# Performance work log

Measured on AMD Instinct MI355X. Metric: run time of the kernel, lower is better.

## Reference

```python
import jax, jax.numpy as jnp
import numpy as np

N_COMP = 16  # sedenion components

def _cd_table(n):
    """Cayley-Dickson basis multiplication table: e_i * e_j = sign[i,j] * e_{idx[i,j]}."""
    if n == 1:
        return np.array([[1]], dtype=np.int64), np.array([[0]], dtype=np.int64)
    m = n // 2
    s, k = _cd_table(m)
    conj = np.where(np.arange(m) == 0, 1, -1)  # conj(e_0)=e_0, conj(e_i)=-e_i
    S = np.zeros((n, n), dtype=np.int64)
    K = np.zeros((n, n), dtype=np.int64)
    for i in range(n):
        for j in range(n):
            if i < m and j < m:          # (a,0)(c,0) = (ac, 0)
                S[i, j] = s[i, j]; K[i, j] = k[i, j]
            elif i < m:                  # (a,0)(0,d) = (0, d a)
                q = j - m
                S[i, j] = s[q, i]; K[i, j] = m + k[q, i]
            elif j < m:                  # (0,b)(c,0) = (0, b c*)
                p = i - m
                S[i, j] = s[p, j] * conj[j]; K[i, j] = m + k[p, j]
            else:                        # (0,b)(0,d) = (-d* b, 0)
                p, q = i - m, j - m
                S[i, j] = -conj[q] * s[q, p]; K[i, j] = k[q, p]
    return S, K

SIGN, IDX = _cd_table(N_COMP)

def _sedenion_kernel(w_comp):
    """Assemble the (16n, 16n) real matrix of the sedenion linear map from 16 (n,n) component weights."""
    blocks = [[None] * N_COMP for _ in range(N_COMP)]
    for i in range(N_COMP):
        for j in range(N_COMP):
            blocks[j][int(IDX[i, j])] = float(SIGN[i, j]) * w_comp[i]
    return jnp.concatenate([jnp.concatenate(row, axis=1) for row in blocks], axis=0)


def setup_inputs() -> dict:
    key = jax.random.key(0)
    k1, k2, k3, k4 = jax.random.split(key, 4)
    B, C, H, W = 8, 96, 256, 256
    x = jax.random.normal(k1, (B, C, H, W), jnp.float32)
    w_comp = jax.random.normal(k2, (N_COMP, C, C), jnp.float32) * 0.02
    proj_w = jax.random.normal(k3, (C, C), jnp.float32) * 0.02
    proj_b = jax.random.normal(k4, (C,), jnp.float32) * 0.02
    return {"x": x, "w_comp": w_comp, "proj_w": proj_w, "proj_b": proj_b}


def reference(x, w_comp, proj_w, proj_b):
    B, C, H, W = x.shape
    h, w = H // 4, W // 4
    # get_window: 'b c (h s1) (w s2) -> b h w (s1 s2 c)' with s1=s2=4
    xw = x.reshape(B, C, h, 4, w, 4).transpose(0, 2, 4, 3, 5, 1).reshape(B, h, w, 16 * C)
    big = _sedenion_kernel(w_comp)          # (16C, 16C)
    y = xw @ big                            # sedenion linear on windowed features
    # reverse_window + 'b c h w -> b h w c' fused: (B,h,w,16C) -> (B,H,W,C)
    y = y.reshape(B, h, w, 4, 4, C).transpose(0, 1, 3, 2, 4, 5).reshape(B, H, W, C)
    y = jax.nn.gelu(y, approximate=False)   # nn.GELU (exact); dropouts are identity (p=0)
    y = y @ proj_w.T + proj_b               # nn.Linear(dim, dim)
    return y.transpose(0, 3, 1, 2)          # 'b h w c -> b c h w'
```

## Files before the change

kernel.cpp:

```cpp
#include <hip/hip_runtime.h>
#include <hip/hip_bf16.h>

typedef __attribute__((ext_vector_type(8))) short short8v;
typedef __attribute__((ext_vector_type(4))) float float4v;

struct SedTab { signed char sgn[256]; signed char idx[256]; };

__device__ inline unsigned short f2bf(float f) {
    __hip_bfloat16 h = __float2bfloat16(f);
    return *reinterpret_cast<unsigned short*>(&h);
}
__device__ inline float bf2f(unsigned short u) {
    union { unsigned int i; float f; } x; x.i = ((unsigned)u) << 16; return x.f;
}

#define GLOAD_LDS16(g, l) __builtin_amdgcn_global_load_lds( \
    (const __attribute__((address_space(1))) void*)(g), \
    (__attribute__((address_space(3))) void*)(l), 16, 0, 0)

#define VMCNT(n) asm volatile("s_waitcnt vmcnt(" #n ")" ::: "memory")

__global__ __launch_bounds__(256) void build_bigT(
    const float* __restrict__ w_comp, unsigned short* __restrict__ bigT, SedTab tab)
{
    int e = blockIdx.x * 256 + threadIdx.x;
    if (e >= 1536 * 1536) return;
    int n = e / 1536, k = e - n * 1536;
    int t_out = n / 96, c = n - t_out * 96;
    int t_in = k / 96, m = k - t_in * 96;
    int i = tab.idx[t_in * 16 + t_out];
    float s = (float)tab.sgn[t_in * 16 + t_out];
    float v = s * w_comp[(i * 96 + m) * 96 + c];
    bigT[e] = f2bf(v);
}

__global__ __launch_bounds__(256) void window_cast(
    const float* __restrict__ x, unsigned short* __restrict__ xw)
{
    __shared__ unsigned short lds[96][260];
    int blk = blockIdx.x;
    int s1 = blk & 3, hh = (blk >> 2) & 63, b = blk >> 8;
    const float* src = x + (size_t)b * 6291456 + (size_t)(4 * hh + s1) * 256;

    for (int i = threadIdx.x; i < 6144; i += 256) {
        int m = i >> 6;
        int q = (i & 63) << 2;
        float4 v = *(const float4*)(src + (size_t)m * 65536 + q);
        lds[m][q + 0] = f2bf(v.x);
        lds[m][q + 1] = f2bf(v.y);
        lds[m][q + 2] = f2bf(v.z);
        lds[m][q + 3] = f2bf(v.w);
    }
    __syncthreads();
    size_t rowbase = (size_t)((b * 64 + hh) * 64) * 1536 + (size_t)s1 * 384;
    for (int i = threadIdx.x; i < 3072; i += 256) {
        int ww = i / 48, g = i - ww * 48;
        int s2 = g / 12, mg = (g - s2 * 12) * 8;
        int qq = 4 * ww + s2;
        short8v pk;
        #pragma unroll
        for (int j = 0; j < 8; ++j) pk[j] = (short)lds[mg + j][qq];
        *(short8v*)(xw + rowbase + (size_t)ww * 1536 + s2 * 96 + mg) = pk;
    }
}

__global__ __launch_bounds__(512, 2) void gemm_sed8(
    const unsigned short* __restrict__ A,
    const unsigned short* __restrict__ Bt,
    unsigned short* __restrict__ Yg)
{
    __shared__ unsigned short As[3][256 * 64];
    __shared__ unsigned short Bs[2][256 * 64];
    const int t = threadIdx.x;
    const int lane = t & 63, w = t >> 6;
    const int wm = w >> 2, wn = w & 3;
    const int lr = lane & 15, lg = lane >> 4;

    const int bid = blockIdx.x;
    const int wg = (bid & 7) * 96 + (bid >> 3);
    const int nt = wg >> 7, mt = wg & 127;
    const int m0 = mt * 256, n0 = nt * 256;

    float4v acc[8][4];
    #pragma unroll
    for (int i = 0; i < 8; ++i)
        #pragma unroll
        for (int j = 0; j < 4; ++j) acc[i][j] = (float4v)0.0f;

    const int r0c = t >> 3,          r1c = (t + 512) >> 3;
    const int kc0 = ((t & 7) ^ (r0c & 7)) << 3;
    const int kc1 = (((t + 512) & 7) ^ (r1c & 7)) << 3;
    const unsigned short* gA0 = A  + (size_t)(m0 + r0c) * 1536 + kc0;
    const unsigned short* gA1 = A  + (size_t)(m0 + r1c) * 1536 + kc1;
    const unsigned short* gB0 = Bt + (size_t)(n0 + r0c) * 1536 + kc0;
    const unsigned short* gB1 = Bt + (size_t)(n0 + r1c) * 1536 + kc1;
    const int d0 = t * 16, d1 = (t + 512) * 16;

    auto stage2 = [&](const unsigned short* g0, const unsigned short* g1,
                      char* ldst, int ko, int half) {
        GLOAD_LDS16(g0 + ko + half * 196608, ldst + half * 16384 + d0);
        GLOAD_LDS16(g1 + ko + half * 196608, ldst + half * 16384 + d1);
    };

    char* a_rd = (char*)&As[0][0];
    char* a_md = (char*)&As[0][0] + 32768;
    char* a_wr = (char*)&As[0][0] + 65536;
    char* b_rd = (char*)&Bs[0][0];
    char* b_wr = (char*)&Bs[0][0] + 32768;

    stage2(gA0, gA1, a_rd, 0, 0);  stage2(gA0, gA1, a_rd, 0, 1);
    stage2(gB0, gB1, b_rd, 0, 0);  stage2(gB0, gB1, b_rd, 0, 1);
    stage2(gA0, gA1, a_md, 64, 0); stage2(gA0, gA1, a_md, 64, 1);
    VMCNT(4);
    __builtin_amdgcn_s_barrier();

    const int c0 = (lg * 8) ^ ((lr & 7) << 3);
    const int c1 = (32 + lg * 8) ^ ((lr & 7) << 3);
    const int arow0 = wm * 128 + lr;
    const int brow0 = wn * 64 + lr;

    int koB = 64, koA = 128;

    for (int kt = 0; kt < 24; ++kt) {
        const unsigned short* as = (const unsigned short*)a_rd;
        const unsigned short* bs = (const unsigned short*)b_rd;

        short8v a0[4], b0[4];
        #pragma unroll
        for (int mf = 0; mf < 4; ++mf)
            a0[mf] = *(const short8v*)(as + (arow0 + mf * 16) * 64 + c0);
        #pragma unroll
        for (int nf = 0; nf < 4; ++nf)
            b0[nf] = *(const short8v*)(bs + (brow0 + nf * 16) * 64 + c0);
        __builtin_amdgcn_sched_barrier(0);
        __builtin_amdgcn_s_barrier();
        if (kt < 23) stage2(gB0, gB1, b_wr, koB, 0);
        __builtin_amdgcn_s_setprio(1);
        #pragma unroll
        for (int mf = 0; mf < 4; ++mf)
            #pragma unroll
            for (int nf = 0; nf < 4; ++nf)
                acc[mf][nf] = __builtin_amdgcn_mfma_f32_16x16x32_bf16(
                    a0[mf], b0[nf], acc[mf][nf], 0, 0, 0);
        __builtin_amdgcn_s_setprio(0);

        short8v a1[4];
        #pragma unroll
        for (int mf = 0; mf < 4; ++mf)
            a1[mf] = *(const short8v*)(as + (arow0 + 64 + mf * 16) * 64 + c0);
        __builtin_amdgcn_sched_barrier(0);
        __builtin_amdgcn_s_barrier();
        if (kt < 23) stage2(gB0, gB1, b_wr, koB, 1);
        __builtin_amdgcn_s_setprio(1);
        #pragma unroll
        for (int mf = 0; mf < 4; ++mf)
            #pragma unroll
            for (int nf = 0; nf < 4; ++nf)
                acc[4 + mf][nf] = __builtin_amdgcn_mfma_f32_16x16x32_bf16(
                    a1[mf], b0[nf], acc[4 + mf][nf], 0, 0, 0);
        __builtin_amdgcn_s_setprio(0);

        short8v a2[4], b1[4];
        #pragma unroll
        for (int mf = 0; mf < 4; ++mf)
            a2[mf] = *(const short8v*)(as + (arow0 + mf * 16) * 64 + c1);
        #pragma unroll
        for (int nf = 0; nf < 4; ++nf)
            b1[nf] = *(const short8v*)(bs + (brow0 + nf * 16) * 64 + c1);
        __builtin_amdgcn_sched_barrier(0);
        __builtin_amdgcn_s_barrier();
        if (kt < 22) stage2(gA0, gA1, a_wr, koA, 0);
        __builtin_amdgcn_s_setprio(1);
        #pragma unroll
        for (int mf = 0; mf < 4; ++mf)
            #pragma unroll
            for (int nf = 0; nf < 4; ++nf)
                acc[mf][nf] = __builtin_amdgcn_mfma_f32_16x16x32_bf16(
                    a2[mf], b1[nf], acc[mf][nf], 0, 0, 0);
        __builtin_amdgcn_s_setprio(0);

        short8v a3[4];
        #pragma unroll
        for (int mf = 0; mf < 4; ++mf)
            a3[mf] = *(const short8v*)(as + (arow0 + 64 + mf * 16) * 64 + c1);
        if (kt < 22)       { VMCNT(2); }
        else if (kt == 22) { VMCNT(0); }
        __builtin_amdgcn_sched_barrier(0);
        __builtin_amdgcn_s_barrier();
        if (kt < 22) stage2(gA0, gA1, a_wr, koA, 1);
        __builtin_amdgcn_s_setprio(1);
        #pragma unroll
        for (int mf = 0; mf < 4; ++mf)
            #pragma unroll
            for (int nf = 0; nf < 4; ++nf)
                acc[4 + mf][nf] = __builtin_amdgcn_mfma_f32_16x16x32_bf16(
                    a3[mf], b1[nf], acc[4 + mf][nf], 0, 0, 0);
        __builtin_amdgcn_s_setprio(0);

        char* tmp = a_rd; a_rd = a_md; a_md = a_wr; a_wr = tmp;
        tmp = b_rd; b_rd = b_wr; b_wr = tmp;
        koB += 64; koA += 64;
    }

    #pragma unroll
    for (int mf = 0; mf < 8; ++mf) {
        #pragma unroll
        for (int r = 0; r < 4; ++r) {
            const int gm = m0 + wm * 128 + mf * 16 + lg * 4 + r;
            #pragma unroll
            for (int nf = 0; nf < 4; ++nf) {
                const int gn = n0 + wn * 64 + nf * 16 + lr;
                float v = acc[mf][nf][r];
                float g = 0.5f * v * (1.0f + erff(v * 0.70710678118654752f));
                Yg[(size_t)gm * 1536 + gn] = f2bf(g);
            }
        }
    }
}

__global__ __launch_bounds__(256, 2) void proj_mfma(
    const unsigned short* __restrict__ Yg,
    const float* __restrict__ pw, const float* __restrict__ pb,
    float* __restrict__ out)
{
    __shared__ unsigned short gys[256 * 104];
    __shared__ unsigned short pws[96 * 104];
    __shared__ float pbs[96];

    const int blk = blockIdx.x;
    const int s1 = blk & 3, hh = (blk >> 2) & 63, b = blk >> 8;
    const int t = threadIdx.x;
    const int lane = t & 63, w = t >> 6;
    const int lr = lane & 15;

    for (int i = t; i < 9216; i += 256) {
        int r = i / 96, c = i - r * 96;
        pws[r * 104 + c] = f2bf(pw[i]);
    }
    if (t < 96) pbs[t] = pb[t];

    size_t rowbase = (size_t)((b * 64 + hh) * 64) * 1536 + (size_t)s1 * 384;
    for (int i = t; i < 3072; i += 256) {
        int ww = i / 48, v = i - ww * 48;
        short8v pk = *(const short8v*)(Yg + rowbase + (size_t)ww * 1536 + v * 8);
        int s2 = v / 12;
        int c = (v - s2 * 12) * 8;
        int q = 4 * ww + s2;
        *(short8v*)(&gys[q * 104 + c]) = pk;
    }
    __syncthreads();

    float4v acc[6][4];
    #pragma unroll
    for (int i = 0; i < 6; ++i)
        #pragma unroll
        for (int j = 0; j < 4; ++j) acc[i][j] = (float4v)0.0f;

    #pragma unroll
    for (int ks = 0; ks < 3; ++ks) {
        const int lk = ks * 32 + ((lane >> 4) << 3);
        short8v af[6], bf[4];
        #pragma unroll
        for (int mf = 0; mf < 6; ++mf)
            af[mf] = *(const short8v*)(&pws[(mf * 16 + lr) * 104 + lk]);
        #pragma unroll
        for (int nf = 0; nf < 4; ++nf)
            bf[nf] = *(const short8v*)(&gys[(w * 64 + nf * 16 + lr) * 104 + lk]);
        #pragma unroll
        for (int mf = 0; mf < 6; ++mf)
            #pragma unroll
            for (int nf = 0; nf < 4; ++nf)
                acc[mf][nf] = __builtin_amdgcn_mfma_f32_16x16x32_bf16(
                    af[mf], bf[nf], acc[mf][nf], 0, 0, 0);
    }

    const int p = 4 * hh + s1;
    const size_t obase = (size_t)b * 6291456 + (size_t)p * 256;
    #pragma unroll
    for (int mf = 0; mf < 6; ++mf) {
        #pragma unroll
        for (int r = 0; r < 4; ++r) {
            const int c = mf * 16 + (lane >> 4) * 4 + r;
            const float bias = pbs[c];
            #pragma unroll
            for (int nf = 0; nf < 4; ++nf) {
                const int q = w * 64 + nf * 16 + lr;
                out[obase + (size_t)c * 65536 + q] = acc[mf][nf][r] + bias;
            }
        }
    }
}

static void cd_table(int n, int* S, int* K) {
    if (n == 1) { S[0] = 1; K[0] = 0; return; }
    int m = n / 2;
    int s[64], k[64];
    cd_table(m, s, k);
    for (int i = 0; i < n; ++i) {
        for (int j = 0; j < n; ++j) {
            if (i < m && j < m) { S[i*n+j] = s[i*m+j]; K[i*n+j] = k[i*m+j]; }
            else if (i < m) { int q = j - m; S[i*n+j] = s[q*m+i]; K[i*n+j] = m + k[q*m+i]; }
            else if (j < m) { int p = i - m; int cj = (j == 0) ? 1 : -1;
                              S[i*n+j] = s[p*m+j] * cj; K[i*n+j] = m + k[p*m+j]; }
            else { int p = i - m, q = j - m; int cq = (q == 0) ? 1 : -1;
                   S[i*n+j] = -cq * s[q*m+p]; K[i*n+j] = k[q*m+p]; }
        }
    }
}

extern "C" void kernel_launch(void* const* d_in, const int* in_sizes, int n_in,
                              void* d_out, int out_size, void* d_ws, size_t ws_size,
                              hipStream_t stream) {
    const float* x      = (const float*)d_in[0];
    const float* w_comp = (const float*)d_in[1];
    const float* proj_w = (const float*)d_in[2];
    const float* proj_b = (const float*)d_in[3];
    float* out = (float*)d_out;

    unsigned short* BigT = (unsigned short*)d_ws;
    unsigned short* Yg   = (unsigned short*)((char*)d_ws + 4718592);
    unsigned short* Xw   = (unsigned short*)d_out;

    int S16[256], K16[256];
    cd_table(16, S16, K16);
    SedTab tab;
    for (int i = 0; i < 16; ++i)
        for (int j = 0; j < 16; ++j) {
            int k = K16[i * 16 + j];
            tab.idx[j * 16 + k] = (signed char)i;
            tab.sgn[j * 16 + k] = (signed char)S16[i * 16 + j];
        }

    hipLaunchKernelGGL(build_bigT, dim3(9216), dim3(256), 0, stream, w_comp, BigT, tab);
    hipLaunchKernelGGL(window_cast, dim3(2048), dim3(256), 0, stream, x, Xw);
    hipLaunchKernelGGL(gemm_sed8, dim3(768), dim3(512), 0, stream, Xw, BigT, Yg);
    hipLaunchKernelGGL(proj_mfma, dim3(2048), dim3(256), 0, stream, Yg, proj_w, proj_b, out);
}
```

Baseline: 333.0 us.

## Fuse projection GEMM into sedenion GEMM epilogue with 128x384 tiles

Retiles the main GEMM from 256x256 to 128x384 tiles so that each block owns whole 96-channel groups (four spatial sub-positions). The GELU output then stays in LDS, and the 96x96 projection plus bias runs in the same kernel. This removes the bf16 intermediate Y round-trip through global memory and one kernel launch. The cost is a larger LDS footprint (144KB), a different operand-prefetch schedule, each block reloading proj_w, and the windowed input moving from the output buffer into the workspace.

```diff
diff --git a/kernel.cpp b/kernel.cpp
--- a/kernel.cpp
+++ b/kernel.cpp
@@ -9,9 +9,6 @@
 __device__ inline unsigned short f2bf(float f) {
     __hip_bfloat16 h = __float2bfloat16(f);
     return *reinterpret_cast<unsigned short*>(&h);
-}
-__device__ inline float bf2f(unsigned short u) {
-    union { unsigned int i; float f; } x; x.i = ((unsigned)u) << 16; return x.f;
 }
 
 #define GLOAD_LDS16(g, l) __builtin_amdgcn_global_load_lds( \
@@ -64,137 +61,135 @@
     }
 }
 
-__global__ __launch_bounds__(512, 2) void gemm_sed8(
+__global__ __launch_bounds__(512, 2) void gemm_fused(
     const unsigned short* __restrict__ A,
     const unsigned short* __restrict__ Bt,
-    unsigned short* __restrict__ Yg)
+    const float* __restrict__ pw, const float* __restrict__ pb,
+    float* __restrict__ out)
 {
-    __shared__ unsigned short As[3][256 * 64];
-    __shared__ unsigned short Bs[2][256 * 64];
+    __shared__ __attribute__((aligned(16))) char smem[147456];
     const int t = threadIdx.x;
     const int lane = t & 63, w = t >> 6;
     const int wm = w >> 2, wn = w & 3;
     const int lr = lane & 15, lg = lane >> 4;
 
     const int bid = blockIdx.x;
-    const int wg = (bid & 7) * 96 + (bid >> 3);
-    const int nt = wg >> 7, mt = wg & 127;
-    const int m0 = mt * 256, n0 = nt * 256;
-
-    float4v acc[8][4];
-    #pragma unroll
-    for (int i = 0; i < 8; ++i)
-        #pragma unroll
-        for (int j = 0; j < 4; ++j) acc[i][j] = (float4v)0.0f;
-
-    const int r0c = t >> 3,          r1c = (t + 512) >> 3;
-    const int kc0 = ((t & 7) ^ (r0c & 7)) << 3;
-    const int kc1 = (((t + 512) & 7) ^ (r1c & 7)) << 3;
-    const unsigned short* gA0 = A  + (size_t)(m0 + r0c) * 1536 + kc0;
-    const unsigned short* gA1 = A  + (size_t)(m0 + r1c) * 1536 + kc1;
-    const unsigned short* gB0 = Bt + (size_t)(n0 + r0c) * 1536 + kc0;
-    const unsigned short* gB1 = Bt + (size_t)(n0 + r1c) * 1536 + kc1;
-    const int d0 = t * 16, d1 = (t + 512) * 16;
-
-    auto stage2 = [&](const unsigned short* g0, const unsigned short* g1,
-                      char* ldst, int ko, int half) {
-        GLOAD_LDS16(g0 + ko + half * 196608, ldst + half * 16384 + d0);
-        GLOAD_LDS16(g1 + ko + half * 196608, ldst + half * 16384 + d1);
+    const int wg = (bid & 7) * 128 + (bid >> 3);
+    const int nt = wg >> 8, mt = wg & 255;
+    const int m0 = mt * 128, n0 = nt * 384;
+
+    float4v acc[4][6];
+    #pragma unroll
+    for (int i = 0; i < 4; ++i)
+        #pragma unroll
+        for (int j = 0; j < 6; ++j) acc[i][j] = (float4v)0.0f;
+
+    const int rA = t >> 3;
+    const int kc = ((t & 7) ^ (rA & 7)) << 3;
+    const unsigned short* gA = A  + (size_t)(m0 + rA) * 1536 + kc;
+    const unsigned short* gB = Bt + (size_t)(n0 + rA) * 1536 + kc;
+    const int dst = t * 16;
+
+    auto stageA = [&](char* s, int ko) {
+        GLOAD_LDS16(gA + ko,             s + dst);
+        GLOAD_LDS16(gA + ko + 64 * 1536, s + dst + 8192);
     };
-
-    char* a_rd = (char*)&As[0][0];
-    char* a_md = (char*)&As[0][0] + 32768;
-    char* a_wr = (char*)&As[0][0] + 65536;
-    char* b_rd = (char*)&Bs[0][0];
-    char* b_wr = (char*)&Bs[0][0] + 32768;
-
-    stage2(gA0, gA1, a_rd, 0, 0);  stage2(gA0, gA1, a_rd, 0, 1);
-    stage2(gB0, gB1, b_rd, 0, 0);  stage2(gB0, gB1, b_rd, 0, 1);
-    stage2(gA0, gA1, a_md, 64, 0); stage2(gA0, gA1, a_md, 64, 1);
-    VMCNT(4);
+    auto stageB = [&](char* s, int ko) {
+        #pragma unroll
+        for (int i = 0; i < 6; ++i)
+            GLOAD_LDS16(gB + ko + (size_t)i * 64 * 1536, s + dst + i * 8192);
+    };
+
+    char* a_rd = smem;          char* a_md = smem + 16384; char* a_wr = smem + 32768;
+    char* b_rd = smem + 49152;  char* b_wr = smem + 98304;
+
+    stageA(a_rd, 0); stageB(b_rd, 0); stageA(a_md, 64);
+    VMCNT(2);
     __builtin_amdgcn_s_barrier();
 
     const int c0 = (lg * 8) ^ ((lr & 7) << 3);
     const int c1 = (32 + lg * 8) ^ ((lr & 7) << 3);
-    const int arow0 = wm * 128 + lr;
-    const int brow0 = wn * 64 + lr;
+    const int ar = wm * 64 + lr;
+    const int br = wn * 96 + lr;
+
+    short8v aE[4], aO[4], b0[3], b1[3], b2[3], b3[3];
+    {
+        const unsigned short* as = (const unsigned short*)a_rd;
+        const unsigned short* bs = (const unsigned short*)b_rd;
+        #pragma unroll
+        for (int mf = 0; mf < 4; ++mf) aE[mf] = *(const short8v*)(as + (ar + mf * 16) * 64 + c0);
+        #pragma unroll
+        for (int j = 0; j < 3; ++j)    b0[j]  = *(const short8v*)(bs + (br + j * 16) * 64 + c0);
+        __builtin_amdgcn_sched_barrier(0);
+    }
 
     int koB = 64, koA = 128;
-
     for (int kt = 0; kt < 24; ++kt) {
         const unsigned short* as = (const unsigned short*)a_rd;
         const unsigned short* bs = (const unsigned short*)b_rd;
 
-        short8v a0[4], b0[4];
+        if (kt < 23) stageB(b_wr, koB);
+        __builtin_amdgcn_s_barrier();
+        #pragma unroll
+        for (int j = 0; j < 3; ++j) b1[j] = *(const short8v*)(bs + (br + (3 + j) * 16) * 64 + c0);
+        __builtin_amdgcn_sched_barrier(0);
+        __builtin_amdgcn_s_setprio(1);
         #pragma unroll
         for (int mf = 0; mf < 4; ++mf)
-            a0[mf] = *(const short8v*)(as + (arow0 + mf * 16) * 64 + c0);
-        #pragma unroll
-        for (int nf = 0; nf < 4; ++nf)
-            b0[nf] = *(const short8v*)(bs + (brow0 + nf * 16) * 64 + c0);
-        __builtin_amdgcn_sched_barrier(0);
+            #pragma unroll
+            for (int nf = 0; nf < 3; ++nf)
+                acc[mf][nf] = __builtin_amdgcn_mfma_f32_16x16x32_bf16(
+                    aE[mf], b0[nf], acc[mf][nf], 0, 0, 0);
+        __builtin_amdgcn_s_setprio(0);
+
         __builtin_amdgcn_s_barrier();
-        if (kt < 23) stage2(gB0, gB1, b_wr, koB, 0);
+        #pragma unroll
+        for (int mf = 0; mf < 4; ++mf) aO[mf] = *(const short8v*)(as + (ar + mf * 16) * 64 + c1);
+        #pragma unroll
+        for (int j = 0; j < 3; ++j)    b2[j]  = *(const short8v*)(bs + (br + j * 16) * 64 + c1);
+        __builtin_amdgcn_sched_barrier(0);
         __builtin_amdgcn_s_setprio(1);
         #pragma unroll
         for (int mf = 0; mf < 4; ++mf)
             #pragma unroll
-            for (int nf = 0; nf < 4; ++nf)
+            for (int nf = 0; nf < 3; ++nf)
+                acc[mf][3 + nf] = __builtin_amdgcn_mfma_f32_16x16x32_bf16(
+                    aE[mf], b1[nf], acc[mf][3 + nf], 0, 0, 0);
+        __builtin_amdgcn_s_setprio(0);
+
+        if (kt < 22) stageA(a_wr, koA);
+        __builtin_amdgcn_s_barrier();
+        #pragma unroll
+        for (int j = 0; j < 3; ++j) b3[j] = *(const short8v*)(bs + (br + (3 + j) * 16) * 64 + c1);
+        __builtin_amdgcn_sched_barrier(0);
+        __builtin_amdgcn_s_setprio(1);
+        #pragma unroll
+        for (int mf = 0; mf < 4; ++mf)
+            #pragma unroll
+            for (int nf = 0; nf < 3; ++nf)
                 acc[mf][nf] = __builtin_amdgcn_mfma_f32_16x16x32_bf16(
-                    a0[mf], b0[nf], acc[mf][nf], 0, 0, 0);
+                    aO[mf], b2[nf], acc[mf][nf], 0, 0, 0);
         __builtin_amdgcn_s_setprio(0);
 
-        short8v a1[4];
-        #pragma unroll
-        for (int mf = 0; mf < 4; ++mf)
-            a1[mf] = *(const short8v*)(as + (arow0 + 64 + mf * 16) * 64 + c0);
-        __builtin_amdgcn_sched_barrier(0);
-        __builtin_amdgcn_s_barrier();
-        if (kt < 23) stage2(gB0, gB1, b_wr, koB, 1);
-        __builtin_amdgcn_s_setprio(1);
-        #pragma unroll
-        for (int mf = 0; mf < 4; ++mf)
-            #pragma unroll
-            for (int nf = 0; nf < 4; ++nf)
-                acc[4 + mf][nf] = __builtin_amdgcn_mfma_f32_16x16x32_bf16(
-                    a1[mf], b0[nf], acc[4 + mf][nf], 0, 0, 0);
-        __builtin_amdgcn_s_setprio(0);
-
-        short8v a2[4], b1[4];
-        #pragma unroll
-        for (int mf = 0; mf < 4; ++mf)
-            a2[mf] = *(const short8v*)(as + (arow0 + mf * 16) * 64 + c1);
-        #pragma unroll
-        for (int nf = 0; nf < 4; ++nf)
-            b1[nf] = *(const short8v*)(bs + (brow0 + nf * 16) * 64 + c1);
-        __builtin_amdgcn_sched_barrier(0);
-        __builtin_amdgcn_s_barrier();
-        if (kt < 22) stage2(gA0, gA1, a_wr, koA, 0);
-        __builtin_amdgcn_s_setprio(1);
-        #pragma unroll
-        for (int mf = 0; mf < 4; ++mf)
-            #pragma unroll
-            for (int nf = 0; nf < 4; ++nf)
-                acc[mf][nf] = __builtin_amdgcn_mfma_f32_16x16x32_bf16(
-                    a2[mf], b1[nf], acc[mf][nf], 0, 0, 0);
-        __builtin_amdgcn_s_setprio(0);
-
-        short8v a3[4];
-        #pragma unroll
-        for (int mf = 0; mf < 4; ++mf)
-            a3[mf] = *(const short8v*)(as + (arow0 + 64 + mf * 16) * 64 + c1);
         if (kt < 22)       { VMCNT(2); }
         else if (kt == 22) { VMCNT(0); }
-        __builtin_amdgcn_sched_barrier(0);
         __builtin_amdgcn_s_barrier();
-        if (kt < 22) stage2(gA0, gA1, a_wr, koA, 1);
+        if (kt < 23) {
+            const unsigned short* asn = (const unsigned short*)a_md;
+            const unsigned short* bsn = (const unsigned short*)b_wr;
+            #pragma unroll
+            for (int mf = 0; mf < 4; ++mf) aE[mf] = *(const short8v*)(asn + (ar + mf * 16) * 64 + c0);
+            #pragma unroll
+            for (int j = 0; j < 3; ++j)    b0[j]  = *(const short8v*)(bsn + (br + j * 16) * 64 + c0);
+        }
+        __builtin_amdgcn_sched_barrier(0);
         __builtin_amdgcn_s_setprio(1);
         #pragma unroll
         for (int mf = 0; mf < 4; ++mf)
             #pragma unroll
-            for (int nf = 0; nf < 4; ++nf)
-                acc[4 + mf][nf] = __builtin_amdgcn_mfma_f32_16x16x32_bf16(
-                    a3[mf], b1[nf], acc[4 + mf][nf], 0, 0, 0);
+            for (int nf = 0; nf < 3; ++nf)
+                acc[mf][3 + nf] = __builtin_amdgcn_mfma_f32_16x16x32_bf16(
+                    aO[mf], b3[nf], acc[mf][3 + nf], 0, 0, 0);
         __builtin_amdgcn_s_setprio(0);
 
         char* tmp = a_rd; a_rd = a_md; a_md = a_wr; a_wr = tmp;
@@ -202,90 +197,73 @@
         koB += 64; koA += 64;
     }
 
-    #pragma unroll
-    for (int mf = 0; mf < 8; ++mf) {
+    __syncthreads();
+
+    unsigned short* yl  = (unsigned short*)smem;
+    unsigned short* pwl = (unsigned short*)(smem + 106496);
+    float*          pbl = (float*)(smem + 126464);
+
+    for (int i = t; i < 9216; i += 512) {
+        int r = i / 96, c = i - r * 96;
+        pwl[r * 104 + c] = f2bf(pw[i]);
+    }
+    if (t < 96) pbl[t] = pb[t];
+
+    #pragma unroll
+    for (int mf = 0; mf < 4; ++mf) {
         #pragma unroll
         for (int r = 0; r < 4; ++r) {
-            const int gm = m0 + wm * 128 + mf * 16 + lg * 4 + r;
-            #pragma unroll
-            for (int nf = 0; nf < 4; ++nf) {
-                const int gn = n0 + wn * 64 + nf * 16 + lr;
+            const int ww = mf * 16 + lg * 4 + r;
+            const int pos = wm * 256 + 4 * ww + wn;
+            #pragma unroll
+            for (int nf = 0; nf < 6; ++nf) {
                 float v = acc[mf][nf][r];
                 float g = 0.5f * v * (1.0f + erff(v * 0.70710678118654752f));
-                Yg[(size_t)gm * 1536 + gn] = f2bf(g);
+                yl[pos * 104 + nf * 16 + lr] = f2bf(g);
             }
         }
     }
-}
-
-__global__ __launch_bounds__(256, 2) void proj_mfma(
-    const unsigned short* __restrict__ Yg,
-    const float* __restrict__ pw, const float* __restrict__ pb,
-    float* __restrict__ out)
-{
-    __shared__ unsigned short gys[256 * 104];
-    __shared__ unsigned short pws[96 * 104];
-    __shared__ float pbs[96];
-
-    const int blk = blockIdx.x;
-    const int s1 = blk & 3, hh = (blk >> 2) & 63, b = blk >> 8;
-    const int t = threadIdx.x;
-    const int lane = t & 63, w = t >> 6;
-    const int lr = lane & 15;
-
-    for (int i = t; i < 9216; i += 256) {
-        int r = i / 96, c = i - r * 96;
-        pws[r * 104 + c] = f2bf(pw[i]);
-    }
-    if (t < 96) pbs[t] = pb[t];
-
-    size_t rowbase = (size_t)((b * 64 + hh) * 64) * 1536 + (size_t)s1 * 384;
-    for (int i = t; i < 3072; i += 256) {
-        int ww = i / 48, v = i - ww * 48;
-        short8v pk = *(const short8v*)(Yg + rowbase + (size_t)ww * 1536 + v * 8);
-        int s2 = v / 12;
-        int c = (v - s2 * 12) * 8;
-        int q = 4 * ww + s2;
-        *(short8v*)(&gys[q * 104 + c]) = pk;
-    }
     __syncthreads();
 
-    float4v acc[6][4];
+    float4v pacc[6][4];
     #pragma unroll
     for (int i = 0; i < 6; ++i)
         #pragma unroll
-        for (int j = 0; j < 4; ++j) acc[i][j] = (float4v)0.0f;
-
+        for (int j = 0; j < 4; ++j) pacc[i][j] = (float4v)0.0f;
+
+    const int posr = w * 64 + lr;
     #pragma unroll
     for (int ks = 0; ks < 3; ++ks) {
-        const int lk = ks * 32 + ((lane >> 4) << 3);
-        short8v af[6], bf[4];
-        #pragma unroll
-        for (int mf = 0; mf < 6; ++mf)
-            af[mf] = *(const short8v*)(&pws[(mf * 16 + lr) * 104 + lk]);
-        #pragma unroll
-        for (int nf = 0; nf < 4; ++nf)
-            bf[nf] = *(const short8v*)(&gys[(w * 64 + nf * 16 + lr) * 104 + lk]);
-        #pragma unroll
-        for (int mf = 0; mf < 6; ++mf)
-            #pragma unroll
-            for (int nf = 0; nf < 4; ++nf)
-                acc[mf][nf] = __builtin_amdgcn_mfma_f32_16x16x32_bf16(
-                    af[mf], bf[nf], acc[mf][nf], 0, 0, 0);
-    }
-
-    const int p = 4 * hh + s1;
+        const int ck = ks * 32 + lg * 8;
+        short8v pf[6], yf[4];
+        #pragma unroll
+        for (int mf2 = 0; mf2 < 6; ++mf2)
+            pf[mf2] = *(const short8v*)(pwl + (mf2 * 16 + lr) * 104 + ck);
+        #pragma unroll
+        for (int nf2 = 0; nf2 < 4; ++nf2)
+            yf[nf2] = *(const short8v*)(yl + (posr + nf2 * 16) * 104 + ck);
+        #pragma unroll
+        for (int mf2 = 0; mf2 < 6; ++mf2)
+            #pragma unroll
+            for (int nf2 = 0; nf2 < 4; ++nf2)
+                pacc[mf2][nf2] = __builtin_amdgcn_mfma_f32_16x16x32_bf16(
+                    pf[mf2], yf[nf2], pacc[mf2][nf2], 0, 0, 0);
+    }
+
+    const int b  = mt >> 5;
+    const int hh = (mt & 31) * 2 + (w >> 2);
+    const int p  = 4 * hh + nt;
     const size_t obase = (size_t)b * 6291456 + (size_t)p * 256;
     #pragma unroll
-    for (int mf = 0; mf < 6; ++mf) {
+    for (int mf2 = 0; mf2 < 6; ++mf2) {
         #pragma unroll
         for (int r = 0; r < 4; ++r) {
-            const int c = mf * 16 + (lane >> 4) * 4 + r;
-            const float bias = pbs[c];
-            #pragma unroll
-            for (int nf = 0; nf < 4; ++nf) {
-                const int q = w * 64 + nf * 16 + lr;
-                out[obase + (size_t)c * 65536 + q] = acc[mf][nf][r] + bias;
+            const int co = mf2 * 16 + lg * 4 + r;
+            const float bias = pbl[co];
+            #pragma unroll
+            for (int nf2 = 0; nf2 < 4; ++nf2) {
+                const int q = (w & 3) * 64 + nf2 * 16 + lr;
+                out[obase + (size_t)co * 65536 + q] = pacc[mf2][nf2][r] + bias;
             }
         }
     }
@@ -317,9 +295,8 @@
     const float* proj_b = (const float*)d_in[3];
     float* out = (float*)d_out;
 
-    unsigned short* BigT = (unsigned short*)d_ws;
-    unsigned short* Yg   = (unsigned short*)((char*)d_ws + 4718592);
-    unsigned short* Xw   = (unsigned short*)d_out;
+    unsigned short* Xw   = (unsigned short*)d_ws;
+    unsigned short* BigT = (unsigned short*)((char*)d_ws + 100663296);
 
     int S16[256], K16[256];
     cd_table(16, S16, K16);
@@ -333,6 +310,6 @@
 
     hipLaunchKernelGGL(build_bigT, dim3(9216), dim3(256), 0, stream, w_comp, BigT, tab);
     hipLaunchKernelGGL(window_cast, dim3(2048), dim3(256), 0, stream, x, Xw);
-    hipLaunchKernelGGL(gemm_sed8, dim3(768), dim3(512), 0, stream, Xw, BigT, Yg);
-    hipLaunchKernelGGL(proj_mfma, dim3(2048), dim3(256), 0, stream, Yg, proj_w, proj_b, out);
-}
+    hipLaunchKernelGGL(gemm_fused, dim3(1024), dim3(512), 0, stream,
+                       Xw, BigT, proj_w, proj_b, out);
+}
```

Result: faster. 302.2 us (-9.3%).
